# Optimization experiments

Measured on AMD Instinct MI355X. Metric: run time of the kernel, lower is better.

Reference implementation:

```python
import jax, jax.numpy as jnp
import numpy as np

N = 100000      # nodes
E = 1600000     # edges (avg degree 16)
D = 128         # in = hid = out dim


def setup_inputs() -> dict:
    key = jax.random.key(0)
    ks = jax.random.split(key, 7)
    x = jax.random.normal(ks[0], (N, D), dtype=jnp.float32)
    src = jax.random.randint(ks[1], (E,), 0, N, dtype=jnp.int32)
    dst = jax.random.randint(ks[2], (E,), 0, N, dtype=jnp.int32)
    s = 1.0 / np.sqrt(2 * D)  # torch Linear default init bound
    W0 = jax.random.uniform(ks[3], (D, 2 * D), jnp.float32, -s, s)
    b0 = jax.random.uniform(ks[4], (D,), jnp.float32, -s, s)
    W1 = jax.random.uniform(ks[5], (D, 2 * D), jnp.float32, -s, s)
    b1 = jax.random.uniform(ks[6], (D,), jnp.float32, -s, s)
    return {"x": x, "src": src, "dst": dst, "W0": W0, "b0": b0, "W1": W1, "b1": b1}


def graph_conv_left(x, src, dst):
    """DGL GraphConv(norm='left', weight=False, bias=False):
    h_v = sum_{(u->v) in E} x_u / max(outdeg(u), 1)."""
    n = x.shape[0]
    deg = jax.ops.segment_sum(jnp.ones_like(src, dtype=x.dtype), src, num_segments=n)
    deg = jnp.maximum(deg, 1.0)
    msgs = (x / deg[:, None])[src]          # [E, D] gather of normalized src feats
    return jax.ops.segment_sum(msgs, dst, num_segments=n)  # [N, D] scatter-add


def reference(x, src, dst, W0, b0, W1, b1):
    # layer 0: concat(self, agg) -> linear -> relu
    h = jnp.concatenate([x, graph_conv_left(x, src, dst)], axis=1)  # [N, 2D]
    h = jax.nn.relu(h @ W0.T + b0)                                  # [N, D]
    # layer 1 (output): concat -> linear (no relu)
    out = jnp.concatenate([h, graph_conv_left(h, src, dst)], axis=1) @ W1.T + b1
    return out
```

## Files before the change

kernel.cpp:

```cpp
#include <hip/hip_runtime.h>
#include <hip/hip_fp16.h>

#define DIM 128
#define CAP 64
#define BW_LOG 9
#define BW_NODES 512
#define MAXNB 256
#define SCAP 10240
#define CHUNK_P 2048
#define CURSTRIDE 16
#define WSTRIDE 264

typedef _Float16 f16x8 __attribute__((ext_vector_type(8)));
typedef float f32x4 __attribute__((ext_vector_type(4)));
typedef unsigned int uint;

__global__ __launch_bounds__(256) void k_prep(const float* __restrict__ W0,
                                              const float* __restrict__ W1,
                                              const float* __restrict__ x,
                                              __half* __restrict__ Wh0,
                                              __half* __restrict__ Wh1,
                                              __half* __restrict__ fh,
                                              uint* __restrict__ curD,
                                              uint* __restrict__ deg,
                                              int NB, int N, int nquadX) {
    int i = blockIdx.x * 256 + threadIdx.x;
    if (i < NB) curD[i * CURSTRIDE] = (uint)i * SCAP;
    if (i < N) deg[i] = 0u;
    const float* in; __half* out; int q;
    if (i < 8192)        { in = W0; out = Wh0; q = i; }
    else if (i < 16384)  { in = W1; out = Wh1; q = i - 8192; }
    else {
        q = i - 16384;
        if (q >= nquadX) return;
        in = x; out = fh;
    }
    float4 v = ((const float4*)in)[q];
    __half2* o = (__half2*)out;
    o[q * 2]     = __floats2half2_rn(v.x, v.y);
    o[q * 2 + 1] = __floats2half2_rn(v.z, v.w);
}

__global__ __launch_bounds__(256) void k_scatter(const int* __restrict__ src,
                                                 const int* __restrict__ dst,
                                                 uint* __restrict__ curD,
                                                 uint* __restrict__ deg,
                                                 uint* __restrict__ dbuf,
                                                 int E, int NB) {
    __shared__ uint cb[MAXNB], bb[MAXNB], rb[MAXNB];
    for (int i = threadIdx.x; i < NB; i += 256) { cb[i] = 0; rb[i] = 0; }
    __syncthreads();
    int e0 = blockIdx.x * CHUNK_P;
    int e1 = min(e0 + CHUNK_P, E);

    int4 sv[2], dv[2];
    bool ok[2];

#pragma unroll
    for (int q = 0; q < 2; ++q) {
        int i4 = (e0 >> 2) + q * 256 + (int)threadIdx.x;
        int e = i4 << 2;
        ok[q] = (e < e1);
        if (ok[q]) {
            sv[q] = ((const int4*)src)[i4];
            dv[q] = ((const int4*)dst)[i4];
            atomicAdd(&cb[dv[q].x >> BW_LOG], 1);
            atomicAdd(&cb[dv[q].y >> BW_LOG], 1);
            atomicAdd(&cb[dv[q].z >> BW_LOG], 1);
            atomicAdd(&cb[dv[q].w >> BW_LOG], 1);
        }
    }
    __syncthreads();
    for (int i = threadIdx.x; i < NB; i += 256)
        if (cb[i]) bb[i] = atomicAdd(&curD[i * CURSTRIDE], cb[i]);
    __syncthreads();
#pragma unroll
    for (int q = 0; q < 2; ++q) {
        if (!ok[q]) continue;
        int ks[4] = {dv[q].x, dv[q].y, dv[q].z, dv[q].w};
        int ps[4] = {sv[q].x, sv[q].y, sv[q].z, sv[q].w};
#pragma unroll
        for (int k = 0; k < 4; ++k) {
            atomicAdd(&deg[ps[k]], 1u);
            uint bkt = (uint)ks[k] >> BW_LOG;
            uint r = atomicAdd(&rb[bkt], 1);
            uint pos = bb[bkt] + r;
            uint pay = ((uint)(ks[k] & (BW_NODES - 1)) << 17) | (uint)ps[k];
            if (pos < (bkt + 1) * SCAP) dbuf[pos] = pay;
        }
    }
}

__global__ __launch_bounds__(512) void k_build(const uint* __restrict__ dbuf,
                                               const uint* __restrict__ curD,
                                               const uint* __restrict__ deg,
                                               int* __restrict__ edge_pad,
                                               int* __restrict__ cnt,
                                               float* __restrict__ invd,
                                               int N) {
    __shared__ uint cur[BW_NODES];
    for (int i = threadIdx.x; i < BW_NODES; i += 512) cur[i] = 0;
    __syncthreads();
    int b = blockIdx.x;
    uint base = (uint)b * SCAP;
    uint total = curD[b * CURSTRIDE] - base;
    if (total > SCAP) total = SCAP;
    int node0 = b << BW_LOG;
    for (uint i = threadIdx.x; i < total; i += 512) {
        uint v = dbuf[base + i];
        uint local = v >> 17;
        uint s = v & 0x1FFFFu;
        uint slot = atomicAdd(&cur[local], 1);
        if (slot < CAP)
            edge_pad[(size_t)(node0 + (int)local) * CAP + slot] = (int)s;
    }
    __syncthreads();
    for (int i = threadIdx.x; i < BW_NODES; i += 512) {
        int node = node0 + i;
        if (node < N) {
            cnt[node] = (int)(cur[i] < CAP ? cur[i] : CAP);
            uint d = deg[node];
            invd[node] = 1.0f / (float)(d > 1u ? d : 1u);
        }
    }
}

__global__ __launch_bounds__(256) void k_gather(const __half* __restrict__ feat,
                                                const float* __restrict__ invd,
                                                const int* __restrict__ edge_pad,
                                                const int* __restrict__ cnt_arr,
                                                __half* __restrict__ agg, int n) {
    int v = blockIdx.x * 4 + (threadIdx.x >> 6);
    int lane = threadIdx.x & 63;
    int quad = lane >> 4;
    int lq   = lane & 15;
    if (v >= n) return;
    int cnt = cnt_arr[v];
    if (cnt > CAP) cnt = CAP;

    int u_lane = 0;
    float w_lane = 0.f;
    if (lane < cnt) {
        u_lane = edge_pad[(size_t)v * CAP + lane];
        w_lane = invd[u_lane];
    }

    float acc[8] = {0.f, 0.f, 0.f, 0.f, 0.f, 0.f, 0.f, 0.f};
    int cntUp = (cnt + 7) & ~7;
    for (int j = 0; j < cntUp; j += 8) {
        int   ua = __shfl(u_lane, j + quad);
        float wa = __shfl(w_lane, j + quad);
        int   ub = __shfl(u_lane, j + 4 + quad);
        float wb = __shfl(w_lane, j + 4 + quad);
        uint4 ra = *(const uint4*)&feat[(size_t)ua * 128 + lq * 8];
        uint4 rb = *(const uint4*)&feat[(size_t)ub * 128 + lq * 8];
        const __half2* pa = (const __half2*)&ra;
        const __half2* pb = (const __half2*)&rb;
#pragma unroll
        for (int i = 0; i < 4; ++i) {
            float2 fa = __half22float2(pa[i]);
            float2 fb = __half22float2(pb[i]);
            acc[2 * i]     = fmaf(fa.x, wa, acc[2 * i]);
            acc[2 * i + 1] = fmaf(fa.y, wa, acc[2 * i + 1]);
            acc[2 * i]     = fmaf(fb.x, wb, acc[2 * i]);
            acc[2 * i + 1] = fmaf(fb.y, wb, acc[2 * i + 1]);
        }
    }
#pragma unroll
    for (int off = 16; off <= 32; off <<= 1) {
#pragma unroll
        for (int i = 0; i < 8; ++i) acc[i] += __shfl_xor(acc[i], off);
    }
    if (quad == 0) {
        __half2 o[4];
#pragma unroll
        for (int i = 0; i < 4; ++i) o[i] = __floats2half2_rn(acc[2 * i], acc[2 * i + 1]);
        *(uint4*)&agg[(size_t)v * 128 + lq * 8] = *(const uint4*)o;
    }
}

template <bool RELU, bool OUT16>
__global__ __launch_bounds__(256) void k_gemm_f16(const _Float16* __restrict__ A0,
                                                  const _Float16* __restrict__ A1,
                                                  const _Float16* __restrict__ Wh,
                                                  const float* __restrict__ bias,
                                                  float* __restrict__ out32,
                                                  _Float16* __restrict__ out16,
                                                  int n_rows) {
    __shared__ _Float16 Ws[128 * WSTRIDE];
    int tid  = threadIdx.x;
    int wave = tid >> 6;
    int lane = tid & 63;
    int quad = lane >> 4;
    int l16  = lane & 15;
    int m0 = blockIdx.x * 128 + wave * 32;

#pragma unroll
    for (int i = 0; i < 16; ++i) {
        int chunk = i * 256 + tid;
        int r = chunk >> 5;
        int c = (chunk & 31) * 8;
        *(f16x8*)&Ws[r * WSTRIDE + c] = *(const f16x8*)&Wh[r * 256 + c];
    }
    __syncthreads();

    f32x4 acc[2][8] = {};

    int ra = m0 + l16;
    int rb = m0 + 16 + l16;
    size_t r0 = (size_t)(ra < n_rows ? ra : 0);
    size_t r1 = (size_t)(rb < n_rows ? rb : 0);

#pragma unroll
    for (int ks = 0; ks < 8; ++ks) {
        int k0 = ks * 32;
        const _Float16* Ab = (k0 < 128) ? A0 : A1;
        int kk = (k0 & 127) + quad * 8;
        f16x8 a0 = *(const f16x8*)&Ab[r0 * 128 + kk];
        f16x8 a1 = *(const f16x8*)&Ab[r1 * 128 + kk];
        f16x8 b[8];
#pragma unroll
        for (int t = 0; t < 8; ++t)
            b[t] = *(const f16x8*)&Ws[(t * 16 + l16) * WSTRIDE + k0 + quad * 8];
#pragma unroll
        for (int t = 0; t < 8; ++t) {
            acc[0][t] = __builtin_amdgcn_mfma_f32_16x16x32_f16(a0, b[t], acc[0][t], 0, 0, 0);
            acc[1][t] = __builtin_amdgcn_mfma_f32_16x16x32_f16(a1, b[t], acc[1][t], 0, 0, 0);
        }
    }

#pragma unroll
    for (int t = 0; t < 8; ++t) {
        int col = t * 16 + l16;
        float bv = bias[col];
#pragma unroll
        for (int g = 0; g < 2; ++g) {
#pragma unroll
            for (int r = 0; r < 4; ++r) {
                int row = m0 + g * 16 + quad * 4 + r;
                if (row < n_rows) {
                    float v = acc[g][t][r] + bv;
                    if (RELU) v = fmaxf(v, 0.f);
                    if (OUT16) out16[(size_t)row * 128 + col] = (_Float16)v;
                    else       out32[(size_t)row * 128 + col] = v;
                }
            }
        }
    }
}

extern "C" void kernel_launch(void* const* d_in, const int* in_sizes, int n_in,
                              void* d_out, int out_size, void* d_ws, size_t ws_size,
                              hipStream_t stream) {
    const float* x  = (const float*)d_in[0];
    const int*   src = (const int*)d_in[1];
    const int*   dst = (const int*)d_in[2];
    const float* W0 = (const float*)d_in[3];
    const float* b0 = (const float*)d_in[4];
    const float* W1 = (const float*)d_in[5];
    const float* b1 = (const float*)d_in[6];
    int N = in_sizes[0] / DIM;
    int E = in_sizes[1];
    float* out = (float*)d_out;
    int NB = (N + BW_NODES - 1) >> BW_LOG;

    char* p = (char*)d_ws;
    uint* curD = (uint*)p; p += MAXNB * CURSTRIDE * 4;
    uint* deg  = (uint*)p; p += (size_t)N * 4;
    int*   edge_pad = (int*)p;   p += (size_t)N * CAP * 4;
    int*   cnt      = (int*)p;   p += (size_t)N * 4;
    float* invd     = (float*)p; p += (size_t)N * 4;
    char*  uni = p;
    size_t bufSz = (size_t)NB * SCAP * 4;
    size_t uniSz = bufSz > (size_t)N * DIM * 2 ? bufSz : (size_t)N * DIM * 2;
    p += uniSz;
    uint*   dbuf = (uint*)uni;
    __half* aggh = (__half*)uni;
    __half* fh   = (__half*)p; p += (size_t)N * DIM * 2;
    __half* hh   = (__half*)p; p += (size_t)N * DIM * 2;
    __half* Wh0  = (__half*)p; p += 128 * 256 * 2;
    __half* Wh1  = (__half*)p; p += 128 * 256 * 2;
    (void)ws_size; (void)n_in; (void)out_size;

    int nquadX = N * DIM / 4;
    int gP = (16384 + nquadX + 255) / 256;
    k_prep<<<gP, 256, 0, stream>>>(W0, W1, x, Wh0, Wh1, fh, curD, deg, NB, N, nquadX);

    int nchunk = (E + CHUNK_P - 1) / CHUNK_P;
    k_scatter<<<nchunk, 256, 0, stream>>>(src, dst, curD, deg, dbuf, E, NB);
    k_build<<<NB, 512, 0, stream>>>(dbuf, curD, deg, edge_pad, cnt, invd, N);

    int gG = (N + 3) / 4;
    int gM = (N + 127) / 128;

    k_gather<<<gG, 256, 0, stream>>>(fh, invd, edge_pad, cnt, aggh, N);
    k_gemm_f16<true, true><<<gM, 256, 0, stream>>>((const _Float16*)fh, (const _Float16*)aggh,
                                                   (const _Float16*)Wh0, b0,
                                                   nullptr, (_Float16*)hh, N);

    k_gather<<<gG, 256, 0, stream>>>(hh, invd, edge_pad, cnt, aggh, N);
    k_gemm_f16<false, false><<<gM, 256, 0, stream>>>((const _Float16*)hh, (const _Float16*)aggh,
                                                     (const _Float16*)Wh1, b1,
                                                     out, nullptr, N);
}
```

Baseline: 389.9 us.

## Replace global bucket atomics with per-chunk fixed cells and local degree counting

The edge scatter no longer reserves space with global atomics per bucket, and source degrees are no longer counted with per-edge global atomics. Instead each chunk writes into fixed-size cells for each (bucket, chunk) pair, for both dst and src, along with per-cell counts. The build kernel then runs twice as many blocks: one half fills the padded edge lists, the other counts degrees in shared memory. This removes global atomic contention and the deg/curD initialisation, at the cost of sparse cell reads and possible silent truncation if more than KCELL edges in a chunk land in one bucket.

```diff
diff --git a/kernel.cpp b/kernel.cpp
--- a/kernel.cpp
+++ b/kernel.cpp
@@ -6,9 +6,9 @@
 #define BW_LOG 9
 #define BW_NODES 512
 #define MAXNB 256
-#define SCAP 10240
 #define CHUNK_P 2048
-#define CURSTRIDE 16
+#define KCELL 40
+#define MAXCHUNK 1024
 #define WSTRIDE 264
 
 typedef _Float16 f16x8 __attribute__((ext_vector_type(8)));
@@ -21,12 +21,8 @@
                                               __half* __restrict__ Wh0,
                                               __half* __restrict__ Wh1,
                                               __half* __restrict__ fh,
-                                              uint* __restrict__ curD,
-                                              uint* __restrict__ deg,
-                                              int NB, int N, int nquadX) {
+                                              int nquadX) {
     int i = blockIdx.x * 256 + threadIdx.x;
-    if (i < NB) curD[i * CURSTRIDE] = (uint)i * SCAP;
-    if (i < N) deg[i] = 0u;
     const float* in; __half* out; int q;
     if (i < 8192)        { in = W0; out = Wh0; q = i; }
     else if (i < 16384)  { in = W1; out = Wh1; q = i - 8192; }
@@ -43,84 +39,110 @@
 
 __global__ __launch_bounds__(256) void k_scatter(const int* __restrict__ src,
                                                  const int* __restrict__ dst,
-                                                 uint* __restrict__ curD,
-                                                 uint* __restrict__ deg,
                                                  uint* __restrict__ dbuf,
-                                                 int E, int NB) {
-    __shared__ uint cb[MAXNB], bb[MAXNB], rb[MAXNB];
-    for (int i = threadIdx.x; i < NB; i += 256) { cb[i] = 0; rb[i] = 0; }
+                                                 uint* __restrict__ sbuf,
+                                                 uint* __restrict__ cntD,
+                                                 uint* __restrict__ cntS,
+                                                 int E, int NB, int nchunk) {
+    __shared__ uint rbD[MAXNB], rbS[MAXNB];
+    for (int i = threadIdx.x; i < NB; i += 256) { rbD[i] = 0; rbS[i] = 0; }
     __syncthreads();
-    int e0 = blockIdx.x * CHUNK_P;
-    int e1 = min(e0 + CHUNK_P, E);
+    int blk = blockIdx.x;
+    int e0 = blk * CHUNK_P;
 
     int4 sv[2], dv[2];
     bool ok[2];
-
 #pragma unroll
     for (int q = 0; q < 2; ++q) {
         int i4 = (e0 >> 2) + q * 256 + (int)threadIdx.x;
         int e = i4 << 2;
-        ok[q] = (e < e1);
+        ok[q] = (e < E);
         if (ok[q]) {
             sv[q] = ((const int4*)src)[i4];
             dv[q] = ((const int4*)dst)[i4];
-            atomicAdd(&cb[dv[q].x >> BW_LOG], 1);
-            atomicAdd(&cb[dv[q].y >> BW_LOG], 1);
-            atomicAdd(&cb[dv[q].z >> BW_LOG], 1);
-            atomicAdd(&cb[dv[q].w >> BW_LOG], 1);
-        }
-    }
-    __syncthreads();
-    for (int i = threadIdx.x; i < NB; i += 256)
-        if (cb[i]) bb[i] = atomicAdd(&curD[i * CURSTRIDE], cb[i]);
-    __syncthreads();
+        }
+    }
 #pragma unroll
     for (int q = 0; q < 2; ++q) {
         if (!ok[q]) continue;
-        int ks[4] = {dv[q].x, dv[q].y, dv[q].z, dv[q].w};
-        int ps[4] = {sv[q].x, sv[q].y, sv[q].z, sv[q].w};
+        int ds[4] = {dv[q].x, dv[q].y, dv[q].z, dv[q].w};
+        int ss[4] = {sv[q].x, sv[q].y, sv[q].z, sv[q].w};
 #pragma unroll
         for (int k = 0; k < 4; ++k) {
-            atomicAdd(&deg[ps[k]], 1u);
-            uint bkt = (uint)ks[k] >> BW_LOG;
-            uint r = atomicAdd(&rb[bkt], 1);
-            uint pos = bb[bkt] + r;
-            uint pay = ((uint)(ks[k] & (BW_NODES - 1)) << 17) | (uint)ps[k];
-            if (pos < (bkt + 1) * SCAP) dbuf[pos] = pay;
-        }
+            uint d = (uint)ds[k], s = (uint)ss[k];
+            uint bd = d >> BW_LOG;
+            uint r = atomicAdd(&rbD[bd], 1);
+            if (r < KCELL)
+                dbuf[(bd * (uint)nchunk + (uint)blk) * KCELL + r] =
+                    ((d & (BW_NODES - 1)) << 17) | s;
+            uint bs = s >> BW_LOG;
+            uint r2 = atomicAdd(&rbS[bs], 1);
+            if (r2 < KCELL)
+                sbuf[(bs * (uint)nchunk + (uint)blk) * KCELL + r2] = s;
+        }
+    }
+    __syncthreads();
+    for (int i = threadIdx.x; i < NB; i += 256) {
+        uint cd = rbD[i], cs = rbS[i];
+        cntD[(uint)i * nchunk + blk] = cd < KCELL ? cd : KCELL;
+        cntS[(uint)i * nchunk + blk] = cs < KCELL ? cs : KCELL;
     }
 }
 
 __global__ __launch_bounds__(512) void k_build(const uint* __restrict__ dbuf,
-                                               const uint* __restrict__ curD,
-                                               const uint* __restrict__ deg,
+                                               const uint* __restrict__ cntD,
+                                               const uint* __restrict__ sbuf,
+                                               const uint* __restrict__ cntS,
                                                int* __restrict__ edge_pad,
                                                int* __restrict__ cnt,
                                                float* __restrict__ invd,
-                                               int N) {
+                                               int N, int NB, int nchunk) {
     __shared__ uint cur[BW_NODES];
+    __shared__ uint mcell[MAXCHUNK];
+    bool isD = (int)blockIdx.x < NB;
+    int b = isD ? blockIdx.x : blockIdx.x - NB;
+    const uint* buf = isD ? dbuf : sbuf;
+    const uint* cc  = isD ? cntD : cntS;
+
     for (int i = threadIdx.x; i < BW_NODES; i += 512) cur[i] = 0;
+    for (int c = threadIdx.x; c < nchunk; c += 512) mcell[c] = cc[(uint)b * nchunk + c];
     __syncthreads();
-    int b = blockIdx.x;
-    uint base = (uint)b * SCAP;
-    uint total = curD[b * CURSTRIDE] - base;
-    if (total > SCAP) total = SCAP;
+
+    uint base = (uint)b * nchunk * KCELL;
+    int total = nchunk * KCELL;
     int node0 = b << BW_LOG;
-    for (uint i = threadIdx.x; i < total; i += 512) {
-        uint v = dbuf[base + i];
-        uint local = v >> 17;
-        uint s = v & 0x1FFFFu;
-        uint slot = atomicAdd(&cur[local], 1);
-        if (slot < CAP)
-            edge_pad[(size_t)(node0 + (int)local) * CAP + slot] = (int)s;
-    }
-    __syncthreads();
-    for (int i = threadIdx.x; i < BW_NODES; i += 512) {
-        int node = node0 + i;
-        if (node < N) {
-            cnt[node] = (int)(cur[i] < CAP ? cur[i] : CAP);
-            uint d = deg[node];
-            invd[node] = 1.0f / (float)(d > 1u ? d : 1u);
+    if (isD) {
+        for (int s = threadIdx.x; s < total; s += 512) {
+            int c = s / KCELL;
+            int j = s - c * KCELL;
+            if ((uint)j < mcell[c]) {
+                uint v = buf[base + s];
+                uint local = v >> 17;
+                uint slot = atomicAdd(&cur[local], 1);
+                if (slot < CAP)
+                    edge_pad[(size_t)(node0 + (int)local) * CAP + slot] =
+                        (int)(v & 0x1FFFFu);
+            }
+        }
+        __syncthreads();
+        for (int i = threadIdx.x; i < BW_NODES; i += 512) {
+            int node = node0 + i;
+            if (node < N) cnt[node] = (int)(cur[i] < CAP ? cur[i] : CAP);
+        }
+    } else {
+        for (int s = threadIdx.x; s < total; s += 512) {
+            int c = s / KCELL;
+            int j = s - c * KCELL;
+            if ((uint)j < mcell[c])
+                atomicAdd(&cur[buf[base + s] & (BW_NODES - 1)], 1);
+        }
+        __syncthreads();
+        for (int i = threadIdx.x; i < BW_NODES; i += 512) {
+            int node = node0 + i;
+            if (node < N) {
+                uint d = cur[i];
+                invd[node] = 1.0f / (float)(d > 1u ? d : 1u);
+            }
         }
     }
 }
@@ -263,32 +285,39 @@
     int E = in_sizes[1];
     float* out = (float*)d_out;
     int NB = (N + BW_NODES - 1) >> BW_LOG;
+    int nchunk = (E + CHUNK_P - 1) / CHUNK_P;
+    size_t ncell = (size_t)NB * nchunk;
+    size_t cellWords = ncell * KCELL;
 
     char* p = (char*)d_ws;
-    uint* curD = (uint*)p; p += MAXNB * CURSTRIDE * 4;
-    uint* deg  = (uint*)p; p += (size_t)N * 4;
+    uint* cntD = (uint*)p; p += (ncell * 4 + 63) & ~(size_t)63;
+    uint* cntS = (uint*)p; p += (ncell * 4 + 63) & ~(size_t)63;
     int*   edge_pad = (int*)p;   p += (size_t)N * CAP * 4;
-    int*   cnt      = (int*)p;   p += (size_t)N * 4;
-    float* invd     = (float*)p; p += (size_t)N * 4;
+    int*   cnt      = (int*)p;   p += ((size_t)N * 4 + 63) & ~(size_t)63;
+    float* invd     = (float*)p; p += ((size_t)N * 4 + 63) & ~(size_t)63;
     char*  uni = p;
-    size_t bufSz = (size_t)NB * SCAP * 4;
-    size_t uniSz = bufSz > (size_t)N * DIM * 2 ? bufSz : (size_t)N * DIM * 2;
-    p += uniSz;
+    size_t featB = (size_t)N * DIM * 2;
+    size_t cellB = cellWords * 4;
+    size_t uniSz = cellB > featB ? cellB : featB;
+    p += (uniSz + 63) & ~(size_t)63;
     uint*   dbuf = (uint*)uni;
     __half* aggh = (__half*)uni;
-    __half* fh   = (__half*)p; p += (size_t)N * DIM * 2;
-    __half* hh   = (__half*)p; p += (size_t)N * DIM * 2;
+    __half* fh   = (__half*)p; p += featB;
+    char*  uni2 = p; p += (uniSz + 63) & ~(size_t)63;
+    uint*   sbuf = (uint*)uni2;
+    __half* hh   = (__half*)uni2;
     __half* Wh0  = (__half*)p; p += 128 * 256 * 2;
     __half* Wh1  = (__half*)p; p += 128 * 256 * 2;
     (void)ws_size; (void)n_in; (void)out_size;
 
     int nquadX = N * DIM / 4;
     int gP = (16384 + nquadX + 255) / 256;
-    k_prep<<<gP, 256, 0, stream>>>(W0, W1, x, Wh0, Wh1, fh, curD, deg, NB, N, nquadX);
-
-    int nchunk = (E + CHUNK_P - 1) / CHUNK_P;
-    k_scatter<<<nchunk, 256, 0, stream>>>(src, dst, curD, deg, dbuf, E, NB);
-    k_build<<<NB, 512, 0, stream>>>(dbuf, curD, deg, edge_pad, cnt, invd, N);
+    k_prep<<<gP, 256, 0, stream>>>(W0, W1, x, Wh0, Wh1, fh, nquadX);
+
+    k_scatter<<<nchunk, 256, 0, stream>>>(src, dst, dbuf, sbuf, cntD, cntS,
+                                          E, NB, nchunk);
+    k_build<<<2 * NB, 512, 0, stream>>>(dbuf, cntD, sbuf, cntS,
+                                        edge_pad, cnt, invd, N, NB, nchunk);
 
     int gG = (N + 3) / 4;
     int gM = (N + 127) / 128;
```

Result: faster. 360.0 us (-7.7%).
